# Kernel optimization log

Measured on AMD Instinct MI355X. Metric: run time of the kernel, lower is better.

Reference implementation:

```python
import jax, jax.numpy as jnp
import numpy as np

EMB, HID = 256, 516
VX, VY = 32000, 32000
SRC, TGT, B = 64, 65, 32


def _lstm_cell(xt, h, c, Wih, Whh, b):
    # PyTorch gate order: i, f, g, o
    gates = xt @ Wih.T + h @ Whh.T + b  # [B, 4H]
    i, f, g, o = jnp.split(gates, 4, axis=-1)
    c = jax.nn.sigmoid(f) * c + jax.nn.sigmoid(i) * jnp.tanh(g)
    h = jax.nn.sigmoid(o) * jnp.tanh(c)
    return h, c


def setup_inputs() -> dict:
    key = jax.random.key(0)
    ks = jax.random.split(key, 32)
    s = 0.05
    n = lambda k, shp: (jax.random.normal(k, shp, jnp.float32) * s)
    inp = {
        "x": jax.random.randint(ks[0], (SRC, B), 0, VX),
        "y": jax.random.randint(ks[1], (TGT, B), 0, VY),
        "encemb": n(ks[2], (VX, EMB)),
        "decemb": n(ks[3], (VX, EMB)),  # sized from vocab_x, as in original
        "enc_Wih0": n(ks[4], (4 * HID, EMB)),
        "enc_Whh0": n(ks[5], (4 * HID, HID)),
        "enc_bih0": n(ks[6], (4 * HID,)),
        "enc_bhh0": n(ks[7], (4 * HID,)),
        "enc_Wih1": n(ks[8], (4 * HID, HID)),
        "enc_Whh1": n(ks[9], (4 * HID, HID)),
        "enc_bih1": n(ks[10], (4 * HID,)),
        "enc_bhh1": n(ks[11], (4 * HID,)),
        "dec_Wih0": n(ks[12], (4 * HID, EMB)),
        "dec_Whh0": n(ks[13], (4 * HID, HID)),
        "dec_bih0": n(ks[14], (4 * HID,)),
        "dec_bhh0": n(ks[15], (4 * HID,)),
        "dec_Wih1": n(ks[16], (4 * HID, HID)),
        "dec_Whh1": n(ks[17], (4 * HID, HID)),
        "dec_bih1": n(ks[18], (4 * HID,)),
        "dec_bhh1": n(ks[19], (4 * HID,)),
        "Wout": n(ks[20], (VY, HID)),
        "bout": n(ks[21], (VY,)),
    }
    return inp


def reference(x, y, encemb, decemb,
              enc_Wih0, enc_Whh0, enc_bih0, enc_bhh0,
              enc_Wih1, enc_Whh1, enc_bih1, enc_bhh1,
              dec_Wih0, dec_Whh0, dec_bih0, dec_bhh0,
              dec_Wih1, dec_Whh1, dec_bih1, dec_bhh1,
              Wout, bout):
    Bn = x.shape[1]
    z = jnp.zeros((Bn, HID), jnp.float32)
    be0 = enc_bih0 + enc_bhh0
    be1 = enc_bih1 + enc_bhh1
    bd0 = dec_bih0 + dec_bhh0
    bd1 = dec_bih1 + dec_bhh1

    # ---- encoder: 2-layer LSTM over embedded source (dropout = identity/eval) ----
    e_x = encemb[x]  # [S, B, E]

    def enc_step(carry, xt):
        h0, c0, h1, c1 = carry
        h0, c0 = _lstm_cell(xt, h0, c0, enc_Wih0, enc_Whh0, be0)
        h1, c1 = _lstm_cell(h0, h1, c1, enc_Wih1, enc_Whh1, be1)
        return (h0, c0, h1, c1), None

    carry, _ = jax.lax.scan(enc_step, (z, z, z, z), e_x)

    # ---- decoder: per-step teacher-forced decode + summed per-step mean CE ----
    def dec_step(carry, ys):
        yt, ytn = ys  # current token [B], next token [B]
        h0, c0, h1, c1 = carry
        xt = decemb[yt]  # [B, E]
        h0, c0 = _lstm_cell(xt, h0, c0, dec_Wih0, dec_Whh0, bd0)
        h1, c1 = _lstm_cell(h0, h1, c1, dec_Wih1, dec_Whh1, bd1)
        logits = h1 @ Wout.T + bout  # [B, V]
        logp = jax.nn.log_softmax(logits, axis=-1)
        step_loss = -jnp.mean(jnp.take_along_axis(logp, ytn[:, None], axis=1))
        return (h0, c0, h1, c1), step_loss

    _, losses = jax.lax.scan(dec_step, carry, (y[:-1], y[1:]))
    return jnp.sum(losses)
```

## Files before the change

### kernel.cpp

```cpp
#include <hip/hip_runtime.h>

typedef __attribute__((ext_vector_type(8))) short short8;
typedef __attribute__((ext_vector_type(4))) float f32x4;
typedef unsigned long long ull;

constexpr int H    = 516;
constexpr int GP   = 2080;
constexpr int KH   = 544;
constexpr int KE   = 256;
constexpr int NB   = 65;
constexpr int SB   = 32;
constexpr int SEQ  = 64;
constexpr int MROW = 2048;
constexpr int V    = 32000;
constexpr int NBN  = 250;
constexpr int HSROW = 552;

__device__ __forceinline__ float bf2f(short s) {
  unsigned u = ((unsigned)(unsigned short)s) << 16;
  float f; __builtin_memcpy(&f, &u, 4); return f;
}
__device__ __forceinline__ short f2bf(float f) {
  unsigned u; __builtin_memcpy(&u, &f, 4);
  u += 0x7fffu + ((u >> 16) & 1u);
  return (short)(u >> 16);
}
__device__ __forceinline__ float sigm(float x){ return 1.f/(1.f+__expf(-x)); }
__device__ __forceinline__ float tanh_(float x){ float e=__expf(-2.f*x); return (1.f-e)/(1.f+e); }

__global__ void k_pack_gates(const float* __restrict__ W1, const float* __restrict__ W2,
                             short* __restrict__ dst, int ksteps) {
  int gid = blockIdx.x * 256 + threadIdx.x;
  int total = NB * 2 * ksteps * 64;
  if (gid >= total) return;
  int lane = gid & 63;
  int rest = gid >> 6;
  int ks = rest % ksteps; rest /= ksteps;
  int nt = rest & 1; int bid = rest >> 1;
  int chat = bid * 32 + nt * 16 + (lane & 15);
  int u = chat >> 2, g = chat & 3;
  int kb = ks * 32 + (lane >> 4) * 8;
  short8 v;
#pragma unroll
  for (int j = 0; j < 8; ++j) {
    int k = kb + j;
    const float* src = W1; int kk = k;
    if (k >= KH) { src = W2; kk = k - KH; }
    float f = 0.f;
    if (u < H && kk < H) f = src[(size_t)(g * H + u) * H + kk];
    v[j] = f2bf(f);
  }
  *(short8*)(dst + (size_t)gid * 8) = v;
}

__global__ void k_pack_wout(const float* __restrict__ Wout, short* __restrict__ dst) {
  int gid = blockIdx.x * 256 + threadIdx.x;
  if (gid >= V * (KH / 8)) return;
  int row = gid / (KH / 8);
  int kb = (gid % (KH / 8)) * 8;
  short8 v;
#pragma unroll
  for (int j = 0; j < 8; ++j) {
    int k = kb + j;
    v[j] = f2bf(k < H ? Wout[(size_t)row * H + k] : 0.f);
  }
  *(short8*)(dst + (size_t)gid * 8) = v;
}

__global__ void k_pack_wih(const float* __restrict__ Wih0, short* __restrict__ dst) {
  int gid = blockIdx.x * 256 + threadIdx.x;
  if (gid >= GP * (KE / 8)) return;
  int chat = gid / (KE / 8);
  int kb = (gid % (KE / 8)) * 8;
  int u = chat >> 2, g = chat & 3;
  short8 v;
#pragma unroll
  for (int j = 0; j < 8; ++j)
    v[j] = f2bf(u < H ? Wih0[(size_t)(g * H + u) * KE + kb + j] : 0.f);
  *(short8*)(dst + (size_t)gid * 8) = v;
}

__global__ void k_pack_bias(const float* ebih0, const float* ebhh0, const float* ebih1, const float* ebhh1,
                            const float* dbih0, const float* dbhh0, const float* dbih1, const float* dbhh1,
                            float* b0e, float* b1e, float* b0d, float* b1d) {
  int chat = blockIdx.x * 256 + threadIdx.x;
  if (chat >= GP) return;
  int u = chat >> 2, g = chat & 3, n = g * H + u;
  bool ok = (u < H);
  b0e[chat] = ok ? ebih0[n] + ebhh0[n] : 0.f;
  b1e[chat] = ok ? ebih1[n] + ebhh1[n] : 0.f;
  b0d[chat] = ok ? dbih0[n] + dbhh0[n] : 0.f;
  b1d[chat] = ok ? dbih1[n] + dbhh1[n] : 0.f;
}

__global__ void __launch_bounds__(256) k_embproj(const short* __restrict__ WihP,
                                                 const float* __restrict__ emb,
                                                 const int* __restrict__ toks,
                                                 const float* __restrict__ b0P,
                                                 float* __restrict__ X0P) {
  int tid = threadIdx.x, w = tid >> 6, lane = tid & 63, q = lane >> 4, col = lane & 15;
  int mt = blockIdx.x;
  int ntile = blockIdx.y * 4 + w;
  int tb = ntile * 16 + col;
  int tok = toks[tb];
  const short* Ap = WihP + (size_t)(mt * 16 + col) * KE + q * 8;
  const float* Bp = emb + (size_t)tok * KE + q * 8;
  f32x4 acc = {0.f, 0.f, 0.f, 0.f};
#pragma unroll
  for (int ks = 0; ks < 8; ++ks) {
    short8 a = *(const short8*)(Ap + ks * 32);
    const f32x4* b4 = (const f32x4*)(Bp + ks * 32);
    f32x4 b0v = b4[0], b1v = b4[1];
    short8 bb;
    bb[0]=f2bf(b0v[0]); bb[1]=f2bf(b0v[1]); bb[2]=f2bf(b0v[2]); bb[3]=f2bf(b0v[3]);
    bb[4]=f2bf(b1v[0]); bb[5]=f2bf(b1v[1]); bb[6]=f2bf(b1v[2]); bb[7]=f2bf(b1v[3]);
    acc = __builtin_amdgcn_mfma_f32_16x16x32_bf16(a, bb, acc, 0, 0, 0);
  }
  int chat0 = mt * 16 + q * 4;
  f32x4 bias = *(const f32x4*)(b0P + chat0);
  int t = tb >> 5, b = tb & 31;
  float* dst = X0P + ((size_t)t * GP) * 32 + b;
#pragma unroll
  for (int r = 0; r < 4; ++r)
    dst[(size_t)(chat0 + r) * 32] = acc[r] + bias[r];
}

struct RecArgs {
  const short *WAe, *WBe, *WAd, *WBd;
  const float *X0e, *X0d, *b1e, *b1d;
  short *hst, *H1P;
  unsigned *bar;
};

__global__ void __launch_bounds__(256) k_recur(RecArgs A) {
  const int tid = threadIdx.x, lane = tid & 63, w = tid >> 6;
  const int q = lane >> 4, col = lane & 15;
  const int mt = w >> 1, nt = w & 1;
  const int bid = blockIdx.x;
  const int chat_l = nt * 16 + col, chat = bid * 32 + chat_l;
  const int am = mt * 16 + col;
  __shared__ __align__(16) short hs[2][32][HSROW];
  __shared__ float c0[32][8], c1[32][8];
  __shared__ float gbuf0[32][33], gbuf1[32][33];
  const int tl = tid & 127, cb = tl >> 2, up = tl & 3;
  if (tid < 128) { c0[cb][up * 2] = 0.f; c0[cb][up * 2 + 1] = 0.f; }
  else           { c1[cb][up * 2] = 0.f; c1[cb][up * 2 + 1] = 0.f; }

  short* hsflat = &hs[0][0][0];
  int loff[17];
#pragma unroll
  for (int j = 0; j < 17; ++j) {
    int c = tid + 256 * j;
    int L = (c >= 2176) ? 1 : 0;
    int cc = c - L * 2176;
    int row = cc / 68, kc = cc - row * 68;
    loff[j] = (L * 32 + row) * HSROW + kc * 8;
  }

  for (int i = 0; i < 129; ++i) {
    const int rp = (i + 1) & 1, wp = i & 1;

    const char* gsrc = (const char*)A.hst + (size_t)rp * 69632 + tid * 16;
    short8 tmp[17];
#pragma unroll
    for (int j = 0; j < 17; ++j)
      asm volatile("global_load_dwordx4 %0, %1, off sc0 sc1"
                   : "=v"(tmp[j]) : "v"(gsrc + j * 4096) : "memory");
    asm volatile("s_waitcnt vmcnt(0)" ::: "memory");
#pragma unroll
    for (int j = 0; j < 17; ++j)
      *(short8*)(hsflat + loff[j]) = tmp[j];
    __syncthreads();

    const int ph0 = (i < 128) ? (i >> 6) : 1;
    const int i1 = i - 1;
    const int ph1 = (i >= 1) ? (i1 >> 6) : 0;
    const short* WA = (ph0 ? A.WAd : A.WAe) + (size_t)bid * 17408 + (size_t)(nt * 17 * 64 + lane) * 8;
    const short* WB = (ph1 ? A.WBd : A.WBe) + (size_t)bid * 34816 + (size_t)(nt * 34 * 64 + lane) * 8;
    f32x4 acc0 = {0.f, 0.f, 0.f, 0.f}, acc1 = {0.f, 0.f, 0.f, 0.f};
#pragma unroll
    for (int ks = 0; ks < 17; ++ks) {
      short8 a0 = *(const short8*)&hs[0][am][ks * 32 + q * 8];
      short8 a1 = *(const short8*)&hs[1][am][ks * 32 + q * 8];
      short8 w0 = *(const short8*)(WA + ks * 512);
      short8 w1 = *(const short8*)(WB + ks * 512);
      short8 w2 = *(const short8*)(WB + (size_t)(17 + ks) * 512);
      acc0 = __builtin_amdgcn_mfma_f32_16x16x32_bf16(a0, w0, acc0, 0, 0, 0);
      acc1 = __builtin_amdgcn_mfma_f32_16x16x32_bf16(a0, w1, acc1, 0, 0, 0);
      acc1 = __builtin_amdgcn_mfma_f32_16x16x32_bf16(a1, w2, acc1, 0, 0, 0);
    }
    {
      const float* X0 = ph0 ? A.X0d : A.X0e;
      const int t0 = i & 63;
      f32x4 xv = *(const f32x4*)(X0 + ((size_t)t0 * GP + chat) * 32 + mt * 16 + q * 4);
      const float* b1 = ph1 ? A.b1d : A.b1e;
      float b1v = b1[chat];
#pragma unroll
      for (int r = 0; r < 4; ++r) {
        gbuf0[mt * 16 + q * 4 + r][chat_l] = acc0[r] + xv[r];
        gbuf1[mt * 16 + q * 4 + r][chat_l] = acc1[r] + b1v;
      }
    }
    __syncthreads();

    if (tid < 128) {
      if (i < 128) {
        unsigned hv = 0;
#pragma unroll
        for (int s = 0; s < 2; ++s) {
          int base = up * 8 + s * 4;
          float gi = gbuf0[cb][base + 0], gf = gbuf0[cb][base + 1];
          float gg = gbuf0[cb][base + 2], go = gbuf0[cb][base + 3];
          float c = c0[cb][up * 2 + s];
          float cn = sigm(gf) * c + sigm(gi) * tanh_(gg);
          float hn = sigm(go) * tanh_(cn);
          c0[cb][up * 2 + s] = cn;
          hv |= ((unsigned)(unsigned short)f2bf(hn)) << (16 * s);
        }
        __hip_atomic_store((unsigned*)A.hst + wp * 17408 + cb * 272 + bid * 4 + up, hv,
                           __ATOMIC_RELAXED, __HIP_MEMORY_SCOPE_AGENT);
      }
    } else {
      if (i >= 1) {
        unsigned hv = 0;
#pragma unroll
        for (int s = 0; s < 2; ++s) {
          int base = up * 8 + s * 4;
          float gi = gbuf1[cb][base + 0], gf = gbuf1[cb][base + 1];
          float gg = gbuf1[cb][base + 2], go = gbuf1[cb][base + 3];
          float c = c1[cb][up * 2 + s];
          float cn = sigm(gf) * c + sigm(gi) * tanh_(gg);
          float hn = sigm(go) * tanh_(cn);
          c1[cb][up * 2 + s] = cn;
          hv |= ((unsigned)(unsigned short)f2bf(hn)) << (16 * s);
        }
        __hip_atomic_store((unsigned*)A.hst + wp * 17408 + 8704 + cb * 272 + bid * 4 + up, hv,
                           __ATOMIC_RELAXED, __HIP_MEMORY_SCOPE_AGENT);
        if (i1 >= 64)
          *((unsigned*)A.H1P + (size_t)((i1 - 64) * SB + cb) * 272 + bid * 4 + up) = hv;
      }
    }

    if (i < 128) {
      asm volatile("s_waitcnt vmcnt(0)" ::: "memory");
      __syncthreads();
      if (tid == 0)
        __hip_atomic_store(A.bar + bid * 16, (unsigned)(i + 1),
                           __ATOMIC_RELAXED, __HIP_MEMORY_SCOPE_AGENT);
      if (tid < 64) {
        const unsigned tgt = (unsigned)(i + 1);
        unsigned* p1 = A.bar + lane * 16;
        unsigned* p2 = A.bar + (lane + 1) * 16;
        while (true) {
          unsigned a = __hip_atomic_load(p1, __ATOMIC_RELAXED, __HIP_MEMORY_SCOPE_AGENT);
          unsigned b = __hip_atomic_load(p2, __ATOMIC_RELAXED, __HIP_MEMORY_SCOPE_AGENT);
          if (__all((a >= tgt) && (b >= tgt))) break;
        }
      }
      __syncthreads();
    }
  }
}

__global__ void __launch_bounds__(256) k_project(const short* __restrict__ H1P,
                                                 const short* __restrict__ WoutP,
                                                 const float* __restrict__ bout,
                                                 float* __restrict__ partials) {
  int bM = blockIdx.x, bN = blockIdx.y;
  int tid = threadIdx.x, w = tid >> 6, lane = tid & 63, q = lane >> 4, col = lane & 15;
  int wm = w >> 1, wn = w & 1;
  __shared__ __align__(16) short As[128 * 32];
  __shared__ __align__(16) short Bs[128 * 32];
  __shared__ float sred[128][2];
  f32x4 acc[4][4];
#pragma unroll
  for (int mi = 0; mi < 4; ++mi)
#pragma unroll
    for (int ni = 0; ni < 4; ++ni) acc[mi][ni] = (f32x4){0.f, 0.f, 0.f, 0.f};

  for (int ks = 0; ks < 17; ++ks) {
#pragma unroll
    for (int i = 0; i < 2; ++i) {
      int chunk = tid * 2 + i;
      int row = chunk >> 2, ch = chunk & 3;
      ((short8*)As)[chunk] = *(const short8*)(H1P  + (size_t)(bM * 128 + row) * KH + ks * 32 + ch * 8);
      ((short8*)Bs)[chunk] = *(const short8*)(WoutP + (size_t)(bN * 128 + row) * KH + ks * 32 + ch * 8);
    }
    __syncthreads();
    short8 af[4], bf[4];
#pragma unroll
    for (int mi = 0; mi < 4; ++mi) af[mi] = *(const short8*)(As + (wm * 64 + mi * 16 + col) * 32 + q * 8);
#pragma unroll
    for (int ni = 0; ni < 4; ++ni) bf[ni] = *(const short8*)(Bs + (wn * 64 + ni * 16 + col) * 32 + q * 8);
#pragma unroll
    for (int mi = 0; mi < 4; ++mi)
#pragma unroll
      for (int ni = 0; ni < 4; ++ni)
        acc[mi][ni] = __builtin_amdgcn_mfma_f32_16x16x32_bf16(af[mi], bf[ni], acc[mi][ni], 0, 0, 0);
    __syncthreads();
  }
  float bias[4];
#pragma unroll
  for (int ni = 0; ni < 4; ++ni) bias[ni] = bout[bN * 128 + wn * 64 + ni * 16 + col];
#pragma unroll
  for (int mi = 0; mi < 4; ++mi) {
#pragma unroll
    for (int r = 0; r < 4; ++r) {
      float s = 0.f;
#pragma unroll
      for (int ni = 0; ni < 4; ++ni) s += __expf(acc[mi][ni][r] + bias[ni]);
      s += __shfl_xor(s, 1, 64); s += __shfl_xor(s, 2, 64);
      s += __shfl_xor(s, 4, 64); s += __shfl_xor(s, 8, 64);
      if (col == 0) sred[wm * 64 + mi * 16 + q * 4 + r][wn] = s;
    }
  }
  __syncthreads();
  if (tid < 128)
    partials[(size_t)(bM * 128 + tid) * NBN + bN] = sred[tid][0] + sred[tid][1];
}

__global__ void __launch_bounds__(256) k_finish(const float* __restrict__ partials,
                                                const short* __restrict__ H1P,
                                                const float* __restrict__ Wout,
                                                const float* __restrict__ bout,
                                                const int* __restrict__ y,
                                                float* __restrict__ out) {
  int tid = threadIdx.x, w = tid >> 6, lane = tid & 63;
  int row = blockIdx.x * 4 + w;
  float s = 0.f;
  for (int j = lane; j < NBN; j += 64) s += partials[(size_t)row * NBN + j];
#pragma unroll
  for (int off = 32; off > 0; off >>= 1) s += __shfl_down(s, off, 64);
  int tok = y[row + 32];
  float d = 0.f;
  for (int k = lane; k < H; k += 64)
    d += bf2f(H1P[(size_t)row * KH + k]) * Wout[(size_t)tok * H + k];
#pragma unroll
  for (int off = 32; off > 0; off >>= 1) d += __shfl_down(d, off, 64);
  __shared__ float bsum[4];
  if (lane == 0) bsum[w] = __logf(s) - (d + bout[tok]);
  __syncthreads();
  if (tid == 0) atomicAdd(out, (bsum[0] + bsum[1] + bsum[2] + bsum[3]) * (1.f / 32.f));
}

extern "C" void kernel_launch(void* const* d_in, const int* in_sizes, int n_in,
                              void* d_out, int out_size, void* d_ws, size_t ws_size,
                              hipStream_t stream) {
  const int*   x      = (const int*)d_in[0];
  const int*   y      = (const int*)d_in[1];
  const float* encemb = (const float*)d_in[2];
  const float* decemb = (const float*)d_in[3];
  const float* eWih0  = (const float*)d_in[4];
  const float* eWhh0  = (const float*)d_in[5];
  const float* ebih0  = (const float*)d_in[6];
  const float* ebhh0  = (const float*)d_in[7];
  const float* eWih1  = (const float*)d_in[8];
  const float* eWhh1  = (const float*)d_in[9];
  const float* ebih1  = (const float*)d_in[10];
  const float* ebhh1  = (const float*)d_in[11];
  const float* dWih0  = (const float*)d_in[12];
  const float* dWhh0  = (const float*)d_in[13];
  const float* dbih0  = (const float*)d_in[14];
  const float* dbhh0  = (const float*)d_in[15];
  const float* dWih1  = (const float*)d_in[16];
  const float* dWhh1  = (const float*)d_in[17];
  const float* dbih1  = (const float*)d_in[18];
  const float* dbhh1  = (const float*)d_in[19];
  const float* Wout   = (const float*)d_in[20];
  const float* bout   = (const float*)d_in[21];
  float* out = (float*)d_out;

  char* wsb = (char*)d_ws;
  size_t off = 0;
  auto alloc = [&](size_t bytes) -> void* {
    void* p = wsb + off;
    off += (bytes + 255) & ~(size_t)255;
    return p;
  };
  short* WoutP = (short*)alloc((size_t)V * KH * 2);
  short* WAe   = (short*)alloc((size_t)NB * 17408 * 2);
  short* WBe   = (short*)alloc((size_t)NB * 34816 * 2);
  short* WAd   = (short*)alloc((size_t)NB * 17408 * 2);
  short* WBd   = (short*)alloc((size_t)NB * 34816 * 2);
  short* WihPe = (short*)alloc((size_t)GP * KE * 2);
  short* WihPd = (short*)alloc((size_t)GP * KE * 2);
  float* b0e   = (float*)alloc(GP * 4);
  float* b1e   = (float*)alloc(GP * 4);
  float* b0d   = (float*)alloc(GP * 4);
  float* b1d   = (float*)alloc(GP * 4);
  float* X0e   = (float*)alloc((size_t)SEQ * GP * SB * 4);
  float* X0d   = (float*)alloc((size_t)SEQ * GP * SB * 4);
  short* hst   = (short*)alloc((size_t)2 * 2 * 32 * KH * 2);
  short* H1P   = (short*)alloc((size_t)MROW * KH * 2);
  float* parts = (float*)alloc((size_t)MROW * NBN * 4);
  unsigned* bar = (unsigned*)alloc(NB * 64);

  hipMemsetAsync(d_out, 0, sizeof(float), stream);
  hipMemsetAsync(hst, 0, (size_t)2 * 2 * 32 * KH * 2, stream);
  hipMemsetAsync(bar, 0, NB * 64, stream);

  k_pack_bias<<<(GP + 255) / 256, 256, 0, stream>>>(ebih0, ebhh0, ebih1, ebhh1,
                                                    dbih0, dbhh0, dbih1, dbhh1,
                                                    b0e, b1e, b0d, b1d);
  k_pack_wih<<<(GP * KE / 8 + 255) / 256, 256, 0, stream>>>(eWih0, WihPe);
  k_pack_wih<<<(GP * KE / 8 + 255) / 256, 256, 0, stream>>>(dWih0, WihPd);
  {
    int totA = NB * 2 * 17 * 64, totB = NB * 2 * 34 * 64;
    k_pack_gates<<<(totA + 255) / 256, 256, 0, stream>>>(eWhh0, eWhh0, WAe, 17);
    k_pack_gates<<<(totB + 255) / 256, 256, 0, stream>>>(eWih1, eWhh1, WBe, 34);
    k_pack_gates<<<(totA + 255) / 256, 256, 0, stream>>>(dWhh0, dWhh0, WAd, 17);
    k_pack_gates<<<(totB + 255) / 256, 256, 0, stream>>>(dWih1, dWhh1, WBd, 34);
  }
  k_pack_wout<<<(V * (KH / 8) + 255) / 256, 256, 0, stream>>>(Wout, WoutP);

  k_embproj<<<dim3(GP / 16, 32), 256, 0, stream>>>(WihPe, encemb, x, b0e, X0e);
  k_embproj<<<dim3(GP / 16, 32), 256, 0, stream>>>(WihPd, decemb, y, b0d, X0d);

  RecArgs ra{WAe, WBe, WAd, WBd, X0e, X0d, b1e, b1d, hst, H1P, bar};
  void* kargs[] = {&ra};
  hipLaunchCooperativeKernel((const void*)k_recur, dim3(NB), dim3(256), kargs, 0, stream);

  k_project<<<dim3(MROW / 128, NBN), 256, 0, stream>>>(H1P, WoutP, bout, parts);
  k_finish<<<MROW / 4, 256, 0, stream>>>(parts, H1P, Wout, bout, y, out);
}
```

Baseline: 1.181 ms.

## Split recurrent step into per-layer barriers to overlap layer0 and layer1 across blocks

Replaces the single grid-wide barrier per step with two barrier words, one per LSTM layer. Each block now runs layer 0, publishes its result, then waits only on layer-1 readiness before running layer 1. The layers share one gate buffer, and bias and weight pointers are hoisted out of the loop. This aims to let layer-0 work of the next step overlap layer-1 work on other blocks and to shorten the critical path. The cost is two spin-waits and two staging passes per step instead of one.

```diff
diff --git a/kernel.cpp b/kernel.cpp
--- a/kernel.cpp
+++ b/kernel.cpp
@@ -141,76 +141,89 @@
   const int am = mt * 16 + col;
   __shared__ __align__(16) short hs[2][32][HSROW];
   __shared__ float c0[32][8], c1[32][8];
-  __shared__ float gbuf0[32][33], gbuf1[32][33];
+  __shared__ float gbuf[32][33];
   const int tl = tid & 127, cb = tl >> 2, up = tl & 3;
-  if (tid < 128) { c0[cb][up * 2] = 0.f; c0[cb][up * 2 + 1] = 0.f; }
-  else           { c1[cb][up * 2] = 0.f; c1[cb][up * 2 + 1] = 0.f; }
-
-  short* hsflat = &hs[0][0][0];
-  int loff[17];
-#pragma unroll
-  for (int j = 0; j < 17; ++j) {
+  if (tid < 128) {
+    c0[cb][up * 2] = 0.f; c0[cb][up * 2 + 1] = 0.f;
+    c1[cb][up * 2] = 0.f; c1[cb][up * 2 + 1] = 0.f;
+  }
+
+  int loff[9];
+#pragma unroll
+  for (int j = 0; j < 9; ++j) {
     int c = tid + 256 * j;
-    int L = (c >= 2176) ? 1 : 0;
-    int cc = c - L * 2176;
-    int row = cc / 68, kc = cc - row * 68;
-    loff[j] = (L * 32 + row) * HSROW + kc * 8;
-  }
-
-  for (int i = 0; i < 129; ++i) {
+    if (c < 2176) { int row = c / 68, kc = c - row * 68; loff[j] = row * HSROW + kc * 8; }
+    else loff[j] = 0;
+  }
+  short* hs0 = &hs[0][0][0];
+  short* hs1 = &hs[1][0][0];
+
+  const float b1ve = A.b1e[chat], b1vd = A.b1d[chat];
+  const short* WAe_p = A.WAe + (size_t)bid * 17408 + (size_t)(nt * 17 * 64 + lane) * 8;
+  const short* WAd_p = A.WAd + (size_t)bid * 17408 + (size_t)(nt * 17 * 64 + lane) * 8;
+  const short* WBe_p = A.WBe + (size_t)bid * 34816 + (size_t)(nt * 34 * 64 + lane) * 8;
+  const short* WBd_p = A.WBd + (size_t)bid * 34816 + (size_t)(nt * 34 * 64 + lane) * 8;
+
+  auto spinwait = [&](int word, unsigned tgt) {
+    if (tid < 64) {
+      unsigned* p1 = A.bar + lane * 16 + word;
+      unsigned* p2 = A.bar + (lane + 1) * 16 + word;
+      while (true) {
+        unsigned a = __hip_atomic_load(p1, __ATOMIC_RELAXED, __HIP_MEMORY_SCOPE_AGENT);
+        unsigned b = __hip_atomic_load(p2, __ATOMIC_RELAXED, __HIP_MEMORY_SCOPE_AGENT);
+        if (__all((a >= tgt) && (b >= tgt))) break;
+      }
+    }
+    __syncthreads();
+  };
+
+  auto stage = [&](const char* gsrc, short* dst) {
+    short8 tmp[9];
+#pragma unroll
+    for (int j = 0; j < 8; ++j)
+      asm volatile("global_load_dwordx4 %0, %1, off sc0 sc1"
+                   : "=v"(tmp[j]) : "v"(gsrc + (tid + 256 * j) * 16) : "memory");
+    if (tid < 128)
+      asm volatile("global_load_dwordx4 %0, %1, off sc0 sc1"
+                   : "=v"(tmp[8]) : "v"(gsrc + (tid + 2048) * 16) : "memory");
+    asm volatile("s_waitcnt vmcnt(0)" ::: "memory");
+#pragma unroll
+    for (int j = 0; j < 8; ++j) *(short8*)(dst + loff[j]) = tmp[j];
+    if (tid < 128) *(short8*)(dst + loff[8]) = tmp[8];
+    __syncthreads();
+  };
+
+  for (int i = 0; i <= 128; ++i) {
     const int rp = (i + 1) & 1, wp = i & 1;
 
-    const char* gsrc = (const char*)A.hst + (size_t)rp * 69632 + tid * 16;
-    short8 tmp[17];
-#pragma unroll
-    for (int j = 0; j < 17; ++j)
-      asm volatile("global_load_dwordx4 %0, %1, off sc0 sc1"
-                   : "=v"(tmp[j]) : "v"(gsrc + j * 4096) : "memory");
-    asm volatile("s_waitcnt vmcnt(0)" ::: "memory");
-#pragma unroll
-    for (int j = 0; j < 17; ++j)
-      *(short8*)(hsflat + loff[j]) = tmp[j];
-    __syncthreads();
-
-    const int ph0 = (i < 128) ? (i >> 6) : 1;
-    const int i1 = i - 1;
-    const int ph1 = (i >= 1) ? (i1 >> 6) : 0;
-    const short* WA = (ph0 ? A.WAd : A.WAe) + (size_t)bid * 17408 + (size_t)(nt * 17 * 64 + lane) * 8;
-    const short* WB = (ph1 ? A.WBd : A.WBe) + (size_t)bid * 34816 + (size_t)(nt * 34 * 64 + lane) * 8;
-    f32x4 acc0 = {0.f, 0.f, 0.f, 0.f}, acc1 = {0.f, 0.f, 0.f, 0.f};
-#pragma unroll
-    for (int ks = 0; ks < 17; ++ks) {
-      short8 a0 = *(const short8*)&hs[0][am][ks * 32 + q * 8];
-      short8 a1 = *(const short8*)&hs[1][am][ks * 32 + q * 8];
-      short8 w0 = *(const short8*)(WA + ks * 512);
-      short8 w1 = *(const short8*)(WB + ks * 512);
-      short8 w2 = *(const short8*)(WB + (size_t)(17 + ks) * 512);
-      acc0 = __builtin_amdgcn_mfma_f32_16x16x32_bf16(a0, w0, acc0, 0, 0, 0);
-      acc1 = __builtin_amdgcn_mfma_f32_16x16x32_bf16(a0, w1, acc1, 0, 0, 0);
-      acc1 = __builtin_amdgcn_mfma_f32_16x16x32_bf16(a1, w2, acc1, 0, 0, 0);
-    }
-    {
-      const float* X0 = ph0 ? A.X0d : A.X0e;
+    if (i > 0) spinwait(0, (unsigned)i);
+    f32x4 xv = {0.f, 0.f, 0.f, 0.f};
+    if (i < 128) {
+      const float* X0 = (i >> 6) ? A.X0d : A.X0e;
       const int t0 = i & 63;
-      f32x4 xv = *(const f32x4*)(X0 + ((size_t)t0 * GP + chat) * 32 + mt * 16 + q * 4);
-      const float* b1 = ph1 ? A.b1d : A.b1e;
-      float b1v = b1[chat];
-#pragma unroll
-      for (int r = 0; r < 4; ++r) {
-        gbuf0[mt * 16 + q * 4 + r][chat_l] = acc0[r] + xv[r];
-        gbuf1[mt * 16 + q * 4 + r][chat_l] = acc1[r] + b1v;
-      }
-    }
-    __syncthreads();
-
-    if (tid < 128) {
-      if (i < 128) {
+      xv = *(const f32x4*)(X0 + ((size_t)t0 * GP + chat) * 32 + mt * 16 + q * 4);
+    }
+    stage((const char*)A.hst + (size_t)rp * 69632, hs0);
+    if (i < 128) {
+      const short* WA = (i >> 6) ? WAd_p : WAe_p;
+      f32x4 acc0 = {0.f, 0.f, 0.f, 0.f};
+#pragma unroll
+      for (int ks = 0; ks < 17; ++ks) {
+        short8 a0 = *(const short8*)&hs[0][am][ks * 32 + q * 8];
+        short8 w0 = *(const short8*)(WA + ks * 512);
+        acc0 = __builtin_amdgcn_mfma_f32_16x16x32_bf16(a0, w0, acc0, 0, 0, 0);
+      }
+#pragma unroll
+      for (int r = 0; r < 4; ++r)
+        gbuf[mt * 16 + q * 4 + r][chat_l] = acc0[r] + xv[r];
+      __syncthreads();
+      if (tid < 128) {
         unsigned hv = 0;
 #pragma unroll
         for (int s = 0; s < 2; ++s) {
           int base = up * 8 + s * 4;
-          float gi = gbuf0[cb][base + 0], gf = gbuf0[cb][base + 1];
-          float gg = gbuf0[cb][base + 2], go = gbuf0[cb][base + 3];
+          float gi = gbuf[cb][base + 0], gf = gbuf[cb][base + 1];
+          float gg = gbuf[cb][base + 2], go = gbuf[cb][base + 3];
           float c = c0[cb][up * 2 + s];
           float cn = sigm(gf) * c + sigm(gi) * tanh_(gg);
           float hn = sigm(go) * tanh_(cn);
@@ -220,14 +233,40 @@
         __hip_atomic_store((unsigned*)A.hst + wp * 17408 + cb * 272 + bid * 4 + up, hv,
                            __ATOMIC_RELAXED, __HIP_MEMORY_SCOPE_AGENT);
       }
-    } else {
-      if (i >= 1) {
+      asm volatile("s_waitcnt vmcnt(0)" ::: "memory");
+      __syncthreads();
+      if (tid == 0)
+        __hip_atomic_store(A.bar + bid * 16, (unsigned)(i + 1),
+                           __ATOMIC_RELAXED, __HIP_MEMORY_SCOPE_AGENT);
+    }
+
+    if (i > 0) spinwait(1, (unsigned)i);
+    stage((const char*)A.hst + (size_t)rp * 69632 + 34816, hs1);
+    if (i >= 1) {
+      const int i1 = i - 1, ph1 = i1 >> 6;
+      const short* WB = ph1 ? WBd_p : WBe_p;
+      const float b1v = ph1 ? b1vd : b1ve;
+      f32x4 acc1 = {0.f, 0.f, 0.f, 0.f};
+#pragma unroll
+      for (int ks = 0; ks < 17; ++ks) {
+        short8 a0 = *(const short8*)&hs[0][am][ks * 32 + q * 8];
+        short8 a1 = *(const short8*)&hs[1][am][ks * 32 + q * 8];
+        short8 w1 = *(const short8*)(WB + ks * 512);
+        short8 w2 = *(const short8*)(WB + (size_t)(17 + ks) * 512);
+        acc1 = __builtin_amdgcn_mfma_f32_16x16x32_bf16(a0, w1, acc1, 0, 0, 0);
+        acc1 = __builtin_amdgcn_mfma_f32_16x16x32_bf16(a1, w2, acc1, 0, 0, 0);
+      }
+#pragma unroll
+      for (int r = 0; r < 4; ++r)
+        gbuf[mt * 16 + q * 4 + r][chat_l] = acc1[r] + b1v;
+      __syncthreads();
+      if (tid < 128) {
         unsigned hv = 0;
 #pragma unroll
         for (int s = 0; s < 2; ++s) {
           int base = up * 8 + s * 4;
-          float gi = gbuf1[cb][base + 0], gf = gbuf1[cb][base + 1];
-          float gg = gbuf1[cb][base + 2], go = gbuf1[cb][base + 3];
+          float gi = gbuf[cb][base + 0], gf = gbuf[cb][base + 1];
+          float gg = gbuf[cb][base + 2], go = gbuf[cb][base + 3];
           float c = c1[cb][up * 2 + s];
           float cn = sigm(gf) * c + sigm(gi) * tanh_(gg);
           float hn = sigm(go) * tanh_(cn);
@@ -239,25 +278,17 @@
         if (i1 >= 64)
           *((unsigned*)A.H1P + (size_t)((i1 - 64) * SB + cb) * 272 + bid * 4 + up) = hv;
       }
-    }
-
-    if (i < 128) {
-      asm volatile("s_waitcnt vmcnt(0)" ::: "memory");
-      __syncthreads();
+      if (i < 128) {
+        asm volatile("s_waitcnt vmcnt(0)" ::: "memory");
+        __syncthreads();
+        if (tid == 0)
+          __hip_atomic_store(A.bar + bid * 16 + 1, (unsigned)(i + 1),
+                             __ATOMIC_RELAXED, __HIP_MEMORY_SCOPE_AGENT);
+      }
+    } else {
       if (tid == 0)
-        __hip_atomic_store(A.bar + bid * 16, (unsigned)(i + 1),
+        __hip_atomic_store(A.bar + bid * 16 + 1, 1u,
                            __ATOMIC_RELAXED, __HIP_MEMORY_SCOPE_AGENT);
-      if (tid < 64) {
-        const unsigned tgt = (unsigned)(i + 1);
-        unsigned* p1 = A.bar + lane * 16;
-        unsigned* p2 = A.bar + (lane + 1) * 16;
-        while (true) {
-          unsigned a = __hip_atomic_load(p1, __ATOMIC_RELAXED, __HIP_MEMORY_SCOPE_AGENT);
-          unsigned b = __hip_atomic_load(p2, __ATOMIC_RELAXED, __HIP_MEMORY_SCOPE_AGENT);
-          if (__all((a >= tgt) && (b >= tgt))) break;
-        }
-      }
-      __syncthreads();
     }
   }
 }
```

Measured after the change: 1.405 ms. 19.0% more time.

## Keep recurrent weights in registers and load hidden state directly into MFMA operands

Applied to the files above, without the earlier changes.

The persistent recurrence kernel now keeps its per-block weight slices resident in VGPRs, loaded once per phase (encoder/decoder) instead of re-read from global memory every timestep. The hidden state is read from global straight into the MFMA A-operand registers, which removes the LDS staging buffer and the __syncthreads that followed it. Unused MFMAs at the boundary steps are skipped and bias/X0 loads are hoisted. This raises register pressure considerably (about 51 short8 weight vectors plus 34 activation vectors per thread), which is why launch bounds are set to one block, and each wave now loads redundant hidden-state rows instead of sharing them through LDS.

```diff
diff --git a/kernel.cpp b/kernel.cpp
--- a/kernel.cpp
+++ b/kernel.cpp
@@ -14,7 +14,6 @@
 constexpr int MROW = 2048;
 constexpr int V    = 32000;
 constexpr int NBN  = 250;
-constexpr int HSROW = 552;
 
 __device__ __forceinline__ float bf2f(short s) {
   unsigned u = ((unsigned)(unsigned short)s) << 16;
@@ -132,69 +131,87 @@
   unsigned *bar;
 };
 
-__global__ void __launch_bounds__(256) k_recur(RecArgs A) {
+__global__ void __launch_bounds__(256, 1) k_recur(RecArgs A) {
   const int tid = threadIdx.x, lane = tid & 63, w = tid >> 6;
   const int q = lane >> 4, col = lane & 15;
   const int mt = w >> 1, nt = w & 1;
   const int bid = blockIdx.x;
   const int chat_l = nt * 16 + col, chat = bid * 32 + chat_l;
   const int am = mt * 16 + col;
-  __shared__ __align__(16) short hs[2][32][HSROW];
   __shared__ float c0[32][8], c1[32][8];
   __shared__ float gbuf0[32][33], gbuf1[32][33];
   const int tl = tid & 127, cb = tl >> 2, up = tl & 3;
   if (tid < 128) { c0[cb][up * 2] = 0.f; c0[cb][up * 2 + 1] = 0.f; }
   else           { c1[cb][up * 2] = 0.f; c1[cb][up * 2 + 1] = 0.f; }
 
-  short* hsflat = &hs[0][0][0];
-  int loff[17];
-#pragma unroll
-  for (int j = 0; j < 17; ++j) {
-    int c = tid + 256 * j;
-    int L = (c >= 2176) ? 1 : 0;
-    int cc = c - L * 2176;
-    int row = cc / 68, kc = cc - row * 68;
-    loff[j] = (L * 32 + row) * HSROW + kc * 8;
-  }
-
-  for (int i = 0; i < 129; ++i) {
+  const float b1ve = A.b1e[chat], b1vd = A.b1d[chat];
+  const short* WAe_p = A.WAe + (size_t)bid * 17408 + (size_t)(nt * 17 * 64 + lane) * 8;
+  const short* WAd_p = A.WAd + (size_t)bid * 17408 + (size_t)(nt * 17 * 64 + lane) * 8;
+  const short* WBe_p = A.WBe + (size_t)bid * 34816 + (size_t)(nt * 34 * 64 + lane) * 8;
+  const short* WBd_p = A.WBd + (size_t)bid * 34816 + (size_t)(nt * 34 * 64 + lane) * 8;
+
+  const char* hb = (const char*)A.hst + (size_t)am * 1088 + q * 16;
+
+  short8 w0[17], w1[17], w2[17];
+
+  for (int i = 0; i <= 128; ++i) {
     const int rp = (i + 1) & 1, wp = i & 1;
 
-    const char* gsrc = (const char*)A.hst + (size_t)rp * 69632 + tid * 16;
-    short8 tmp[17];
-#pragma unroll
-    for (int j = 0; j < 17; ++j)
+    if (i == 0) {
+#pragma unroll
+      for (int ks = 0; ks < 17; ++ks) w0[ks] = *(const short8*)(WAe_p + ks * 512);
+#pragma unroll
+      for (int ks = 0; ks < 17; ++ks) {
+        w1[ks] = *(const short8*)(WBe_p + ks * 512);
+        w2[ks] = *(const short8*)(WBe_p + (size_t)(17 + ks) * 512);
+      }
+    } else if (i == 64) {
+#pragma unroll
+      for (int ks = 0; ks < 17; ++ks) w0[ks] = *(const short8*)(WAd_p + ks * 512);
+    } else if (i == 65) {
+#pragma unroll
+      for (int ks = 0; ks < 17; ++ks) {
+        w1[ks] = *(const short8*)(WBd_p + ks * 512);
+        w2[ks] = *(const short8*)(WBd_p + (size_t)(17 + ks) * 512);
+      }
+    }
+
+    f32x4 xv = {0.f, 0.f, 0.f, 0.f};
+    if (i < 128) {
+      const float* X0 = (i >> 6) ? A.X0d : A.X0e;
+      const int t0 = i & 63;
+      xv = *(const f32x4*)(X0 + ((size_t)t0 * GP + chat) * 32 + mt * 16 + q * 4);
+    }
+
+    const char* h0b = hb + (size_t)rp * 69632;
+    const char* h1b = h0b + 34816;
+    short8 a0[17], a1[17];
+#pragma unroll
+    for (int ks = 0; ks < 17; ++ks)
       asm volatile("global_load_dwordx4 %0, %1, off sc0 sc1"
-                   : "=v"(tmp[j]) : "v"(gsrc + j * 4096) : "memory");
+                   : "=v"(a0[ks]) : "v"(h0b + ks * 64) : "memory");
+#pragma unroll
+    for (int ks = 0; ks < 17; ++ks)
+      asm volatile("global_load_dwordx4 %0, %1, off sc0 sc1"
+                   : "=v"(a1[ks]) : "v"(h1b + ks * 64) : "memory");
     asm volatile("s_waitcnt vmcnt(0)" ::: "memory");
-#pragma unroll
-    for (int j = 0; j < 17; ++j)
-      *(short8*)(hsflat + loff[j]) = tmp[j];
-    __syncthreads();
-
-    const int ph0 = (i < 128) ? (i >> 6) : 1;
-    const int i1 = i - 1;
-    const int ph1 = (i >= 1) ? (i1 >> 6) : 0;
-    const short* WA = (ph0 ? A.WAd : A.WAe) + (size_t)bid * 17408 + (size_t)(nt * 17 * 64 + lane) * 8;
-    const short* WB = (ph1 ? A.WBd : A.WBe) + (size_t)bid * 34816 + (size_t)(nt * 34 * 64 + lane) * 8;
+    __builtin_amdgcn_sched_barrier(0);
+
     f32x4 acc0 = {0.f, 0.f, 0.f, 0.f}, acc1 = {0.f, 0.f, 0.f, 0.f};
-#pragma unroll
-    for (int ks = 0; ks < 17; ++ks) {
-      short8 a0 = *(const short8*)&hs[0][am][ks * 32 + q * 8];
-      short8 a1 = *(const short8*)&hs[1][am][ks * 32 + q * 8];
-      short8 w0 = *(const short8*)(WA + ks * 512);
-      short8 w1 = *(const short8*)(WB + ks * 512);
-      short8 w2 = *(const short8*)(WB + (size_t)(17 + ks) * 512);
-      acc0 = __builtin_amdgcn_mfma_f32_16x16x32_bf16(a0, w0, acc0, 0, 0, 0);
-      acc1 = __builtin_amdgcn_mfma_f32_16x16x32_bf16(a0, w1, acc1, 0, 0, 0);
-      acc1 = __builtin_amdgcn_mfma_f32_16x16x32_bf16(a1, w2, acc1, 0, 0, 0);
+    if (i < 128) {
+#pragma unroll
+      for (int ks = 0; ks < 17; ++ks)
+        acc0 = __builtin_amdgcn_mfma_f32_16x16x32_bf16(a0[ks], w0[ks], acc0, 0, 0, 0);
+    }
+    if (i >= 1) {
+#pragma unroll
+      for (int ks = 0; ks < 17; ++ks) {
+        acc1 = __builtin_amdgcn_mfma_f32_16x16x32_bf16(a0[ks], w1[ks], acc1, 0, 0, 0);
+        acc1 = __builtin_amdgcn_mfma_f32_16x16x32_bf16(a1[ks], w2[ks], acc1, 0, 0, 0);
+      }
     }
     {
-      const float* X0 = ph0 ? A.X0d : A.X0e;
-      const int t0 = i & 63;
-      f32x4 xv = *(const f32x4*)(X0 + ((size_t)t0 * GP + chat) * 32 + mt * 16 + q * 4);
-      const float* b1 = ph1 ? A.b1d : A.b1e;
-      float b1v = b1[chat];
+      const float b1v = ((i >= 1) ? ((i - 1) >> 6) : 0) ? b1vd : b1ve;
 #pragma unroll
       for (int r = 0; r < 4; ++r) {
         gbuf0[mt * 16 + q * 4 + r][chat_l] = acc0[r] + xv[r];
@@ -222,6 +239,7 @@
       }
     } else {
       if (i >= 1) {
+        const int i1 = i - 1;
         unsigned hv = 0;
 #pragma unroll
         for (int s = 0; s < 2; ++s) {
```

Result: slower. 1.371 ms (+16.1%).
